# Kernel tuning notes

Hardware: AMD Instinct MI355X
Metric: run time of the kernel (lower is better)

Reference implementation:

```python
import jax, jax.numpy as jnp
import numpy as np

EPS = 1e-12  # matches torch.nn.functional.normalize default eps


def _l2_normalize(x):
    # F.normalize: x / max(||x||_2, eps), along last dim
    n = jnp.linalg.norm(x, axis=-1, keepdims=True)
    return x / jnp.maximum(n, EPS)


def setup_inputs() -> dict:
    key = jax.random.key(0)
    k_q, k_bank = jax.random.split(key)
    B, n_slots, key_dim = 4096, 32768, 128
    query_keys = jax.random.normal(k_q, (B, key_dim), dtype=jnp.float32)
    bank_k = jax.random.normal(k_bank, (n_slots, key_dim), dtype=jnp.float32)
    return {"query_keys": query_keys, "bank_k": bank_k}


def reference(query_keys, bank_k):
    # cosine similarity = dot product of L2-normalized vectors
    q = _l2_normalize(query_keys.astype(jnp.float32))   # (B, d)
    k = _l2_normalize(bank_k.astype(jnp.float32))       # (n_slots, d)
    sims = jnp.einsum('bd,nd->bn', q, k)                # (B, n_slots)
    return jnp.argmax(sims, axis=-1)                    # top-1 slot id per query
```

## Files before the change

kernel.cpp:

```cpp
#include <hip/hip_runtime.h>
#include <stdint.h>

#define B_Q     4096
#define N_SLOTS 32768
#define KD      128
#define BM      128
#define BN      128
#define NSPLIT  16
#define NCHUNK  (N_SLOTS / NSPLIT)
#define NT_BLK  (NCHUNK / BN)
#define CAND_CAP (1 << 20)
#define LCAP    6144
#define SURV_CAP 65536
#define KPANELS (N_SLOTS / 16)
#define QPANELS (B_Q / 16)

typedef _Float16 f16x8 __attribute__((ext_vector_type(8)));
typedef float    f32x4 __attribute__((ext_vector_type(4)));

__device__ __forceinline__ unsigned int ord_f32(float f) {
    unsigned int u = __float_as_uint(f);
    return (u & 0x80000000u) ? ~u : (u | 0x80000000u);
}
__device__ __forceinline__ float ord_inv(unsigned int u) {
    unsigned int b = (u & 0x80000000u) ? (u & 0x7FFFFFFFu) : ~u;
    return __uint_as_float(b);
}

__device__ __forceinline__ unsigned long long shfl_xor_u64(unsigned long long v, int mask, int width) {
    unsigned int lo = (unsigned int)v, hi = (unsigned int)(v >> 32);
    lo = __shfl_xor(lo, mask, width);
    hi = __shfl_xor(hi, mask, width);
    return ((unsigned long long)hi << 32) | lo;
}

__device__ __forceinline__ float rowmax16(float x) {
    x = fmaxf(x, __int_as_float(__builtin_amdgcn_mov_dpp(__float_as_int(x), 0x128, 0xf, 0xf, true)));
    x = fmaxf(x, __int_as_float(__builtin_amdgcn_mov_dpp(__float_as_int(x), 0x124, 0xf, 0xf, true)));
    x = fmaxf(x, __int_as_float(__builtin_amdgcn_mov_dpp(__float_as_int(x), 0x122, 0xf, 0xf, true)));
    x = fmaxf(x, __int_as_float(__builtin_amdgcn_mov_dpp(__float_as_int(x), 0x121, 0xf, 0xf, true)));
    return x;
}

__global__ void prep_pack(const float* __restrict__ Q, const float* __restrict__ Kb,
                          uint4* __restrict__ qp, uint4* __restrict__ kp,
                          float* __restrict__ mg, float* __restrict__ ik,
                          unsigned int* __restrict__ glb,
                          unsigned long long* __restrict__ best2, int* __restrict__ cnt) {
    const int gid = blockIdx.x * blockDim.x + threadIdx.x;
    if (gid < B_Q) { best2[gid] = 0ull; glb[gid] = 0u; }
    if (gid == 0) { cnt[0] = 0; cnt[1] = 0; cnt[2] = 0; cnt[3] = 0; }

    const int p = blockIdx.x;
    const int t = threadIdx.x;
    const int r = t >> 4, c = t & 15;
    const bool isK = p < KPANELS;
    const int row = isK ? p * 16 + r : (p - KPANELS) * 16 + r;
    const float* src = isK ? Kb : Q;
    const float4* rp = reinterpret_cast<const float4*>(src + (size_t)row * KD);
    const float4 va = rp[c * 2], vb = rp[c * 2 + 1];
    float ss = va.x * va.x + va.y * va.y + va.z * va.z + va.w * va.w
             + vb.x * vb.x + vb.y * vb.y + vb.z * vb.z + vb.w * vb.w;
    #pragma unroll
    for (int m = 8; m; m >>= 1) ss += __shfl_xor(ss, m, 16);
    const float nrm = fmaxf(sqrtf(ss), 1e-12f);
    const float scale = isK ? 1.0f / nrm : 1.0f;
    if (c == 0) {
        if (isK) ik[row] = scale;
        else     mg[row] = nrm * 2.2e-3f;
    }
    unsigned short h[8];
    const float e[8] = {va.x, va.y, va.z, va.w, vb.x, vb.y, vb.z, vb.w};
    #pragma unroll
    for (int i = 0; i < 8; ++i) {
        _Float16 hv = (_Float16)(e[i] * scale);
        __builtin_memcpy(&h[i], &hv, 2);
    }
    uint4 out;
    out.x = (unsigned)h[0] | ((unsigned)h[1] << 16);
    out.y = (unsigned)h[2] | ((unsigned)h[3] << 16);
    out.z = (unsigned)h[4] | ((unsigned)h[5] << 16);
    out.w = (unsigned)h[6] | ((unsigned)h[7] << 16);
    uint4* dst = isK ? kp : qp;
    const int pl = isK ? p : p - KPANELS;
    dst[(size_t)(pl * 4 + (c >> 2)) * 64 + (c & 3) * 16 + r] = out;
}

__global__ __launch_bounds__(512, 4) void pass1_kernel(
    const uint4* __restrict__ qp, const uint4* __restrict__ kp,
    const float* __restrict__ mg_g, unsigned int* __restrict__ glb,
    int* __restrict__ cnt, unsigned long long* __restrict__ recs)
{
    __shared__ unsigned long long lbuf[LCAP];
    __shared__ int lcnt;
    __shared__ int sbase;

    const int bid  = blockIdx.x;
    const int q0   = (bid >> 4) * BM;
    const int n0   = ((bid & 7) * 2 + ((bid >> 3) & 1)) * NCHUNK;
    const int tid  = threadIdx.x;
    const int lane = tid & 63;
    const int w    = tid >> 6;
    const int wr   = w >> 1;
    const int wc   = w & 1;
    const int l15  = lane & 15;
    const int lg   = lane >> 4;

    if (tid == 0) lcnt = 0;
    __syncthreads();

    float L[8], mgv[8];
    #pragma unroll
    for (int e = 0; e < 8; ++e) {
        const int row = q0 + wr * 32 + (e >> 2) * 16 + lg * 4 + (e & 3);
        mgv[e] = mg_g[row];
        const unsigned int g = glb[row];
        L[e] = g ? ord_inv(g) : -3e38f;
    }

    f16x8 aq[2][4];
    #pragma unroll
    for (int i = 0; i < 2; ++i)
        #pragma unroll
        for (int kc = 0; kc < 4; ++kc)
            aq[i][kc] = *(const f16x8*)&qp[(size_t)(((q0 >> 4) + wr * 2 + i) * 4 + kc) * 64 + lane];

    const int pbase = (n0 >> 4) + wc * 4;

    #pragma unroll 1
    for (int t = 0; t < NT_BLK; ++t) {
        const int nb = n0 + t * BN;

        f32x4 acc[2][4];
        #pragma unroll
        for (int i = 0; i < 2; ++i)
            #pragma unroll
            for (int j = 0; j < 4; ++j) {
                acc[i][j][0] = 0.f; acc[i][j][1] = 0.f;
                acc[i][j][2] = 0.f; acc[i][j][3] = 0.f;
            }

        #pragma unroll
        for (int kc = 0; kc < 4; ++kc) {
            f16x8 bh[4];
            #pragma unroll
            for (int j = 0; j < 4; ++j)
                bh[j] = *(const f16x8*)&kp[(size_t)((pbase + t * 8 + j) * 4 + kc) * 64 + lane];
            #pragma unroll
            for (int i = 0; i < 2; ++i)
                #pragma unroll
                for (int j = 0; j < 4; ++j)
                    acc[i][j] = __builtin_amdgcn_mfma_f32_16x16x32_f16(aq[i][kc], bh[j], acc[i][j], 0, 0, 0);
        }

        #pragma unroll
        for (int e = 0; e < 8; ++e) {
            const int i = e >> 2, rr = e & 3;
            const float me = fmaxf(fmaxf(fmaxf(acc[i][0][rr], acc[i][1][rr]),
                                         acc[i][2][rr]), acc[i][3][rr]);
            L[e] = rowmax16(fmaxf(L[e], me));
            const float th = L[e] - mgv[e];
            if (me >= th) {
                const int row = q0 + wr * 32 + i * 16 + lg * 4 + rr;
                #pragma unroll
                for (int j = 0; j < 4; ++j) {
                    const float v = acc[i][j][rr];
                    if (v >= th) {
                        const int n = nb + wc * 64 + j * 16 + l15;
                        const int pos = atomicAdd(&lcnt, 1);
                        if (pos < LCAP)
                            lbuf[pos] = ((unsigned long long)ord_f32(v) << 32)
                                      | (unsigned int)((row << 15) | n);
                    }
                }
            }
        }
    }

    if (l15 == 0) {
        #pragma unroll
        for (int e = 0; e < 8; ++e) {
            const int row = q0 + wr * 32 + (e >> 2) * 16 + lg * 4 + (e & 3);
            atomicMax(&glb[row], ord_f32(L[e]));
        }
    }

    __syncthreads();
    const int total = lcnt;
    const int nout  = total < LCAP ? total : LCAP;
    if (tid == 0) {
        const int base = atomicAdd(&cnt[0], nout);
        sbase = base;
        if (total > LCAP || base + nout > CAND_CAP) atomicOr(&cnt[1], 1);
    }
    __syncthreads();
    for (int c = tid; c < nout; c += 512) {
        const int g = sbase + c;
        if (g < CAND_CAP) recs[g] = lbuf[c];
    }
}

__global__ void filter_kernel(const unsigned long long* __restrict__ recs,
                              const unsigned int* __restrict__ glb,
                              const float* __restrict__ mg_g,
                              int* __restrict__ cnt, unsigned int* __restrict__ surv)
{
    __shared__ unsigned int sb[2048];
    __shared__ int sc, sbase;
    const int tid = threadIdx.x;
    if (tid == 0) sc = 0;
    __syncthreads();

    const int cn = cnt[0];
    const int count = cn < CAND_CAP ? cn : CAND_CAP;
    const int nthr = gridDim.x * blockDim.x;
    for (int c = blockIdx.x * blockDim.x + tid; c < count; c += nthr) {
        const unsigned long long rec = recs[c];
        const unsigned int lo = (unsigned int)rec;
        const int q = (int)(lo >> 15);
        const float s = ord_inv((unsigned int)(rec >> 32));
        const unsigned int g = glb[q];
        const float M = g ? ord_inv(g) : 3e38f;
        if (s >= M - mg_g[q]) {
            const int pos = atomicAdd(&sc, 1);
            if (pos < 2048) sb[pos] = lo;
        }
    }
    __syncthreads();
    const int total = sc;
    const int nout  = total < 2048 ? total : 2048;
    if (tid == 0) {
        const int base = atomicAdd(&cnt[2], nout);
        sbase = base;
        if (total > 2048 || base + nout > SURV_CAP) atomicOr(&cnt[3], 1);
    }
    __syncthreads();
    for (int c = tid; c < nout; c += 256) {
        const int g = sbase + c;
        if (g < SURV_CAP) surv[g] = sb[c];
    }
}

__global__ void rescore_kernel(const float* __restrict__ Q, const float* __restrict__ Kb,
                               const float* __restrict__ ik,
                               const int* __restrict__ cnt, const unsigned int* __restrict__ surv,
                               unsigned long long* __restrict__ best2)
{
    const int lane = threadIdx.x & 63;
    const int l15  = lane & 15;
    const int grp  = lane >> 4;
    const int wid  = (blockIdx.x * blockDim.x + threadIdx.x) >> 6;
    const int nw   = (gridDim.x * blockDim.x) >> 6;
    const int ngrp = nw * 4;
    const int scn  = cnt[2];
    const int scount = scn < SURV_CAP ? scn : SURV_CAP;
    const bool bad = (cnt[1] != 0) || (cnt[3] != 0) || (cnt[0] > CAND_CAP);

    if (!bad) {
        for (int c = wid * 4 + grp; c < scount; c += ngrp) {
            const unsigned int lo = surv[c];
            const int q = (int)(lo >> 15), n = (int)(lo & 32767u);
            const float4* qpr = (const float4*)(Q  + (size_t)q * KD);
            const float4* kpr = (const float4*)(Kb + (size_t)n * KD);
            const float4 qa = qpr[l15 * 2], qb = qpr[l15 * 2 + 1];
            const float4 ka = kpr[l15 * 2], kb = kpr[l15 * 2 + 1];
            float dot = qa.x * ka.x + qa.y * ka.y + qa.z * ka.z + qa.w * ka.w
                      + qb.x * kb.x + qb.y * kb.y + qb.z * kb.z + qb.w * kb.w;
            #pragma unroll
            for (int m = 8; m; m >>= 1) dot += __shfl_xor(dot, m, 16);
            if (l15 == 0) {
                const float v = dot * ik[n];
                const unsigned long long pk =
                    ((unsigned long long)ord_f32(v) << 32) | (unsigned int)(~n);
                atomicMax(&best2[q], pk);
            }
        }
    } else {
        for (int q = wid; q < B_Q; q += nw) {
            const float* qr = Q + (size_t)q * KD;
            unsigned long long pb = 0ull;
            for (int n = lane; n < N_SLOTS; n += 64) {
                const float* kr = Kb + (size_t)n * KD;
                float dot = 0.f;
                for (int d = 0; d < KD; ++d) dot = fmaf(qr[d], kr[d], dot);
                const float v = dot * ik[n];
                const unsigned long long p =
                    ((unsigned long long)ord_f32(v) << 32) | (unsigned int)(~n);
                if (p > pb) pb = p;
            }
            #pragma unroll
            for (int m = 32; m; m >>= 1) {
                const unsigned long long o = shfl_xor_u64(pb, m, 64);
                if (o > pb) pb = o;
            }
            if (lane == 0) atomicMax(&best2[q], pb);
        }
    }
}

__global__ void safety_kernel(const float* __restrict__ Q, const float* __restrict__ Kb,
                              const float* __restrict__ ik,
                              unsigned long long* __restrict__ best2) {
    const int lane = threadIdx.x & 63;
    const int wid  = (blockIdx.x * blockDim.x + threadIdx.x) >> 6;
    const int nw   = (gridDim.x * blockDim.x) >> 6;
    for (int q = wid; q < B_Q; q += nw) {
        if (best2[q] != 0ull) continue;
        const float* qr = Q + (size_t)q * KD;
        unsigned long long pb = 0ull;
        for (int n = lane; n < N_SLOTS; n += 64) {
            const float* kr = Kb + (size_t)n * KD;
            float dot = 0.f;
            for (int d = 0; d < KD; ++d) dot = fmaf(qr[d], kr[d], dot);
            const float v = dot * ik[n];
            const unsigned long long p =
                ((unsigned long long)ord_f32(v) << 32) | (unsigned int)(~n);
            if (p > pb) pb = p;
        }
        #pragma unroll
        for (int m = 32; m; m >>= 1) {
            const unsigned long long o = shfl_xor_u64(pb, m, 64);
            if (o > pb) pb = o;
        }
        if (lane == 0) best2[q] = pb;
    }
}

__global__ void decode_kernel(const unsigned long long* __restrict__ best2,
                              int* __restrict__ out) {
    int i = blockIdx.x * blockDim.x + threadIdx.x;
    if (i < B_Q) out[i] = (int)(~(unsigned int)(best2[i] & 0xFFFFFFFFull));
}

__global__ void fallback_kernel(const float* __restrict__ Q, const float* __restrict__ Kb,
                                int* __restrict__ out) {
    __shared__ float q[KD];
    __shared__ unsigned long long red[256];
    const int b = blockIdx.x;
    for (int i = threadIdx.x; i < KD; i += 256) q[i] = Q[(size_t)b * KD + i];
    __syncthreads();
    unsigned long long pbest = 0ull;
    for (int n = threadIdx.x; n < N_SLOTS; n += 256) {
        const float* kr = Kb + (size_t)n * KD;
        float dot = 0.f, ss = 0.f;
        for (int d = 0; d < KD; ++d) { float kv = kr[d]; dot = fmaf(q[d], kv, dot); ss = fmaf(kv, kv, ss); }
        float v = dot / fmaxf(sqrtf(ss), 1e-12f);
        unsigned long long p = ((unsigned long long)ord_f32(v) << 32) | (unsigned int)(~n);
        if (p > pbest) pbest = p;
    }
    red[threadIdx.x] = pbest; __syncthreads();
    for (int s = 128; s; s >>= 1) {
        if (threadIdx.x < (unsigned)s && red[threadIdx.x + s] > red[threadIdx.x])
            red[threadIdx.x] = red[threadIdx.x + s];
        __syncthreads();
    }
    if (threadIdx.x == 0) out[b] = (int)(~(unsigned int)(red[0] & 0xFFFFFFFFull));
}

extern "C" void kernel_launch(void* const* d_in, const int* in_sizes, int n_in,
                              void* d_out, int out_size, void* d_ws, size_t ws_size,
                              hipStream_t stream) {
    const float* Q  = (const float*)d_in[0];
    const float* Kb = (const float*)d_in[1];
    int* out = (int*)d_out;

    const size_t QP_B = (size_t)B_Q * KD * 2;
    const size_t KP_B = (size_t)N_SLOTS * KD * 2;
    const size_t MG_B = (size_t)B_Q * 4;
    const size_t IK_B = (size_t)N_SLOTS * 4;
    const size_t GL_B = (size_t)B_Q * 4;
    const size_t B2_B = (size_t)B_Q * 8;
    const size_t CNT_B = 256;
    const size_t REC_B = (size_t)CAND_CAP * 8;
    const size_t SV_B  = (size_t)SURV_CAP * 4;
    const size_t NEED = QP_B + KP_B + MG_B + IK_B + GL_B + B2_B + CNT_B + REC_B + SV_B;

    if (ws_size < NEED) {
        fallback_kernel<<<B_Q, 256, 0, stream>>>(Q, Kb, out);
        return;
    }

    char* p = (char*)d_ws;
    uint4*          qp  = (uint4*)p;                     p += QP_B;
    uint4*          kp  = (uint4*)p;                     p += KP_B;
    float*          mg  = (float*)p;                     p += MG_B;
    float*          ik  = (float*)p;                     p += IK_B;
    unsigned int*   glb = (unsigned int*)p;              p += GL_B;
    unsigned long long* best2 = (unsigned long long*)p;  p += B2_B;
    int*            cnt = (int*)p;                       p += CNT_B;
    unsigned long long* recs = (unsigned long long*)p;   p += REC_B;
    unsigned int*   surv = (unsigned int*)p;

    prep_pack<<<KPANELS + QPANELS, 256, 0, stream>>>(Q, Kb, qp, kp, mg, ik, glb, best2, cnt);
    pass1_kernel<<<512, 512, 0, stream>>>(qp, kp, mg, glb, cnt, recs);
    filter_kernel<<<256, 256, 0, stream>>>(recs, glb, mg, cnt, surv);
    rescore_kernel<<<256, 256, 0, stream>>>(Q, Kb, ik, cnt, surv, best2);
    safety_kernel<<<64, 256, 0, stream>>>(Q, Kb, ik, best2);
    decode_kernel<<<B_Q / 256, 256, 0, stream>>>(best2, out);
}
```

Baseline: 90.93 us.

## Fuse filter/rescore and safety/decode kernels; double-buffer K fragment loads in pass1

Merges the filter and rescore stages into one kernel that rescores survivors straight from shared memory, and merges the safety and decode stages so the output is written directly. This drops two kernel launches and the global survivor buffer with its counters. The main MFMA loop now prefetches the next K chunk's fragments into alternating register buffers while the current chunk is multiplied, aiming to hide global load latency. The prefetch uses more registers, and the bad-case fallback now runs through the safety kernel with only 64 blocks, so that rare path is slower.

```diff
diff --git a/kernel.cpp b/kernel.cpp
--- a/kernel.cpp
+++ b/kernel.cpp
@@ -11,7 +11,6 @@
 #define NT_BLK  (NCHUNK / BN)
 #define CAND_CAP (1 << 20)
 #define LCAP    6144
-#define SURV_CAP 65536
 #define KPANELS (N_SLOTS / 16)
 #define QPANELS (B_Q / 16)
 
@@ -49,7 +48,7 @@
                           unsigned long long* __restrict__ best2, int* __restrict__ cnt) {
     const int gid = blockIdx.x * blockDim.x + threadIdx.x;
     if (gid < B_Q) { best2[gid] = 0ull; glb[gid] = 0u; }
-    if (gid == 0) { cnt[0] = 0; cnt[1] = 0; cnt[2] = 0; cnt[3] = 0; }
+    if (gid == 0) { cnt[0] = 0; cnt[1] = 0; }
 
     const int p = blockIdx.x;
     const int t = threadIdx.x;
@@ -127,6 +126,11 @@
 
     const int pbase = (n0 >> 4) + wc * 4;
 
+    f16x8 bhA[4], bhB[4];
+    #pragma unroll
+    for (int j = 0; j < 4; ++j)
+        bhA[j] = *(const f16x8*)&kp[(size_t)((pbase + j) * 4 + 0) * 64 + lane];
+
     #pragma unroll 1
     for (int t = 0; t < NT_BLK; ++t) {
         const int nb = n0 + t * BN;
@@ -142,15 +146,18 @@
 
         #pragma unroll
         for (int kc = 0; kc < 4; ++kc) {
-            f16x8 bh[4];
+            const int nkc = (kc + 1) & 3;
+            const int nt  = (kc == 3) ? ((t + 1 < NT_BLK) ? t + 1 : t) : t;
+            f16x8* nxt = (kc & 1) ? bhA : bhB;
+            const f16x8* cur = (kc & 1) ? bhB : bhA;
             #pragma unroll
             for (int j = 0; j < 4; ++j)
-                bh[j] = *(const f16x8*)&kp[(size_t)((pbase + t * 8 + j) * 4 + kc) * 64 + lane];
+                nxt[j] = *(const f16x8*)&kp[(size_t)((pbase + nt * 8 + j) * 4 + nkc) * 64 + lane];
             #pragma unroll
             for (int i = 0; i < 2; ++i)
                 #pragma unroll
                 for (int j = 0; j < 4; ++j)
-                    acc[i][j] = __builtin_amdgcn_mfma_f32_16x16x32_f16(aq[i][kc], bh[j], acc[i][j], 0, 0, 0);
+                    acc[i][j] = __builtin_amdgcn_mfma_f32_16x16x32_f16(aq[i][kc], cur[j], acc[i][j], 0, 0, 0);
         }
 
         #pragma unroll
@@ -200,13 +207,16 @@
     }
 }
 
-__global__ void filter_kernel(const unsigned long long* __restrict__ recs,
-                              const unsigned int* __restrict__ glb,
-                              const float* __restrict__ mg_g,
-                              int* __restrict__ cnt, unsigned int* __restrict__ surv)
+__global__ void filter_rescore_kernel(const unsigned long long* __restrict__ recs,
+                                      const unsigned int* __restrict__ glb,
+                                      const float* __restrict__ mg_g,
+                                      int* __restrict__ cnt,
+                                      const float* __restrict__ Q, const float* __restrict__ Kb,
+                                      const float* __restrict__ ik,
+                                      unsigned long long* __restrict__ best2)
 {
     __shared__ unsigned int sb[2048];
-    __shared__ int sc, sbase;
+    __shared__ int sc;
     const int tid = threadIdx.x;
     if (tid == 0) sc = 0;
     __syncthreads();
@@ -229,83 +239,46 @@
     __syncthreads();
     const int total = sc;
     const int nout  = total < 2048 ? total : 2048;
-    if (tid == 0) {
-        const int base = atomicAdd(&cnt[2], nout);
-        sbase = base;
-        if (total > 2048 || base + nout > SURV_CAP) atomicOr(&cnt[3], 1);
-    }
-    __syncthreads();
-    for (int c = tid; c < nout; c += 256) {
-        const int g = sbase + c;
-        if (g < SURV_CAP) surv[g] = sb[c];
-    }
-}
-
-__global__ void rescore_kernel(const float* __restrict__ Q, const float* __restrict__ Kb,
-                               const float* __restrict__ ik,
-                               const int* __restrict__ cnt, const unsigned int* __restrict__ surv,
-                               unsigned long long* __restrict__ best2)
-{
-    const int lane = threadIdx.x & 63;
+    if (total > 2048 && tid == 0) atomicOr(&cnt[1], 2);
+
+    const int lane = tid & 63;
     const int l15  = lane & 15;
-    const int grp  = lane >> 4;
-    const int wid  = (blockIdx.x * blockDim.x + threadIdx.x) >> 6;
-    const int nw   = (gridDim.x * blockDim.x) >> 6;
-    const int ngrp = nw * 4;
-    const int scn  = cnt[2];
-    const int scount = scn < SURV_CAP ? scn : SURV_CAP;
-    const bool bad = (cnt[1] != 0) || (cnt[3] != 0) || (cnt[0] > CAND_CAP);
-
-    if (!bad) {
-        for (int c = wid * 4 + grp; c < scount; c += ngrp) {
-            const unsigned int lo = surv[c];
-            const int q = (int)(lo >> 15), n = (int)(lo & 32767u);
-            const float4* qpr = (const float4*)(Q  + (size_t)q * KD);
-            const float4* kpr = (const float4*)(Kb + (size_t)n * KD);
-            const float4 qa = qpr[l15 * 2], qb = qpr[l15 * 2 + 1];
-            const float4 ka = kpr[l15 * 2], kb = kpr[l15 * 2 + 1];
-            float dot = qa.x * ka.x + qa.y * ka.y + qa.z * ka.z + qa.w * ka.w
-                      + qb.x * kb.x + qb.y * kb.y + qb.z * kb.z + qb.w * kb.w;
-            #pragma unroll
-            for (int m = 8; m; m >>= 1) dot += __shfl_xor(dot, m, 16);
-            if (l15 == 0) {
-                const float v = dot * ik[n];
-                const unsigned long long pk =
-                    ((unsigned long long)ord_f32(v) << 32) | (unsigned int)(~n);
-                atomicMax(&best2[q], pk);
-            }
-        }
-    } else {
-        for (int q = wid; q < B_Q; q += nw) {
-            const float* qr = Q + (size_t)q * KD;
-            unsigned long long pb = 0ull;
-            for (int n = lane; n < N_SLOTS; n += 64) {
-                const float* kr = Kb + (size_t)n * KD;
-                float dot = 0.f;
-                for (int d = 0; d < KD; ++d) dot = fmaf(qr[d], kr[d], dot);
-                const float v = dot * ik[n];
-                const unsigned long long p =
-                    ((unsigned long long)ord_f32(v) << 32) | (unsigned int)(~n);
-                if (p > pb) pb = p;
-            }
-            #pragma unroll
-            for (int m = 32; m; m >>= 1) {
-                const unsigned long long o = shfl_xor_u64(pb, m, 64);
-                if (o > pb) pb = o;
-            }
-            if (lane == 0) atomicMax(&best2[q], pb);
-        }
-    }
-}
-
-__global__ void safety_kernel(const float* __restrict__ Q, const float* __restrict__ Kb,
-                              const float* __restrict__ ik,
-                              unsigned long long* __restrict__ best2) {
+    const int grp  = (tid >> 6) * 4 + (lane >> 4);
+    const int ngrp = (blockDim.x >> 6) * 4;
+    for (int c = grp; c < nout; c += ngrp) {
+        const unsigned int lo = sb[c];
+        const int q = (int)(lo >> 15), n = (int)(lo & 32767u);
+        const float4* qpr = (const float4*)(Q  + (size_t)q * KD);
+        const float4* kpr = (const float4*)(Kb + (size_t)n * KD);
+        const float4 qa = qpr[l15 * 2], qb = qpr[l15 * 2 + 1];
+        const float4 ka = kpr[l15 * 2], kb = kpr[l15 * 2 + 1];
+        float dot = qa.x * ka.x + qa.y * ka.y + qa.z * ka.z + qa.w * ka.w
+                  + qb.x * kb.x + qb.y * kb.y + qb.z * kb.z + qb.w * kb.w;
+        #pragma unroll
+        for (int m = 8; m; m >>= 1) dot += __shfl_xor(dot, m, 16);
+        if (l15 == 0) {
+            const float v = dot * ik[n];
+            const unsigned long long pk =
+                ((unsigned long long)ord_f32(v) << 32) | (unsigned int)(~n);
+            atomicMax(&best2[q], pk);
+        }
+    }
+}
+
+__global__ void safety_decode_kernel(const float* __restrict__ Q, const float* __restrict__ Kb,
+                                     const float* __restrict__ ik, const int* __restrict__ cnt,
+                                     const unsigned long long* __restrict__ best2,
+                                     int* __restrict__ out) {
     const int lane = threadIdx.x & 63;
     const int wid  = (blockIdx.x * blockDim.x + threadIdx.x) >> 6;
     const int nw   = (gridDim.x * blockDim.x) >> 6;
+    const bool bad = (cnt[1] != 0) || (cnt[0] > CAND_CAP);
     for (int q = wid; q < B_Q; q += nw) {
-        if (best2[q] != 0ull) continue;
+        const unsigned long long b = best2[q];
+        if (!bad && b != 0ull) {
+            if (lane == 0) out[q] = (int)(~(unsigned int)(b & 0xFFFFFFFFull));
+            continue;
+        }
         const float* qr = Q + (size_t)q * KD;
         unsigned long long pb = 0ull;
         for (int n = lane; n < N_SLOTS; n += 64) {
@@ -322,14 +295,8 @@
             const unsigned long long o = shfl_xor_u64(pb, m, 64);
             if (o > pb) pb = o;
         }
-        if (lane == 0) best2[q] = pb;
-    }
-}
-
-__global__ void decode_kernel(const unsigned long long* __restrict__ best2,
-                              int* __restrict__ out) {
-    int i = blockIdx.x * blockDim.x + threadIdx.x;
-    if (i < B_Q) out[i] = (int)(~(unsigned int)(best2[i] & 0xFFFFFFFFull));
+        if (lane == 0) out[q] = (int)(~(unsigned int)(pb & 0xFFFFFFFFull));
+    }
 }
 
 __global__ void fallback_kernel(const float* __restrict__ Q, const float* __restrict__ Kb,
@@ -372,8 +339,7 @@
     const size_t B2_B = (size_t)B_Q * 8;
     const size_t CNT_B = 256;
     const size_t REC_B = (size_t)CAND_CAP * 8;
-    const size_t SV_B  = (size_t)SURV_CAP * 4;
-    const size_t NEED = QP_B + KP_B + MG_B + IK_B + GL_B + B2_B + CNT_B + REC_B + SV_B;
+    const size_t NEED = QP_B + KP_B + MG_B + IK_B + GL_B + B2_B + CNT_B + REC_B;
 
     if (ws_size < NEED) {
         fallback_kernel<<<B_Q, 256, 0, stream>>>(Q, Kb, out);
@@ -388,13 +354,10 @@
     unsigned int*   glb = (unsigned int*)p;              p += GL_B;
     unsigned long long* best2 = (unsigned long long*)p;  p += B2_B;
     int*            cnt = (int*)p;                       p += CNT_B;
-    unsigned long long* recs = (unsigned long long*)p;   p += REC_B;
-    unsigned int*   surv = (unsigned int*)p;
+    unsigned long long* recs = (unsigned long long*)p;
 
     prep_pack<<<KPANELS + QPANELS, 256, 0, stream>>>(Q, Kb, qp, kp, mg, ik, glb, best2, cnt);
     pass1_kernel<<<512, 512, 0, stream>>>(qp, kp, mg, glb, cnt, recs);
-    filter_kernel<<<256, 256, 0, stream>>>(recs, glb, mg, cnt, surv);
-    rescore_kernel<<<256, 256, 0, stream>>>(Q, Kb, ik, cnt, surv, best2);
-    safety_kernel<<<64, 256, 0, stream>>>(Q, Kb, ik, best2);
-    decode_kernel<<<B_Q / 256, 256, 0, stream>>>(best2, out);
-}
+    filter_rescore_kernel<<<256, 256, 0, stream>>>(recs, glb, mg, cnt, Q, Kb, ik, best2);
+    safety_decode_kernel<<<64, 256, 0, stream>>>(Q, Kb, ik, cnt, best2, out);
+}
```

Result: slower. 136.7 us (+50.3%).
